# Performance work log

Measured on AMD Instinct MI355X. Metric: run time of the kernel, lower is better.

## Reference

```python
import jax, jax.numpy as jnp
import numpy as np
from jax import lax

B, C, H, W = 2, 3, 512, 512
K = 8                 # kernel_size (= value_patch_size)
G = H // K            # token grid = 64
L = G * G             # 4096 tokens
FD = 128              # feature_dim
PD = C * K * K        # 192 rgb patch dim
MD = PD + FD          # 320 matching token dim
DD = 256              # matching_descriptor_dim
TOPK = 16             # attention_top_k (= reranker_top_k)
RH = 128              # reranker hidden
TEMP = 1.0
NEG = -1e9


def _to_tokens(img):
    # [B,C,H,W] -> [B,L,C*K*K], channel-major patch layout (torch unfold order)
    b = img.shape[0]
    x = img.reshape(b, C, G, K, G, K).transpose(0, 2, 4, 1, 3, 5)
    return x.reshape(b, L, PD)


def _from_tokens(tok):
    # inverse of _to_tokens (non-overlapping fold)
    b = tok.shape[0]
    x = tok.reshape(b, G, G, C, K, K).transpose(0, 3, 1, 4, 2, 5)
    return x.reshape(b, C, H, W)


def setup_inputs() -> dict:
    key = jax.random.key(0)
    ks = jax.random.split(key, 9)
    s = lambda d: 1.0 / np.sqrt(d)
    return {
        "image": jax.random.normal(ks[0], (B, C, H, W), jnp.float32),
        "features": jax.random.normal(ks[1], (B, FD, G, G), jnp.float32),
        "token_mask": jax.random.randint(ks[2], (B, L), 0, 2, jnp.int32),
        "W_desc": jax.random.normal(ks[3], (MD, DD), jnp.float32) * s(MD),
        "Wq_rr": jax.random.normal(ks[4], (MD, RH), jnp.float32) * s(MD),
        "Wk_rr": jax.random.normal(ks[5], (MD, RH), jnp.float32) * s(MD),
        "W1": jax.random.normal(ks[6], (2 * RH + 3, RH), jnp.float32) * s(2 * RH + 3),
        "b1": jnp.zeros((RH,), jnp.float32),
        "W2": jax.random.normal(ks[7], (RH, 1), jnp.float32) * s(RH),
        "b2": jnp.zeros((1,), jnp.float32),
    }


def reference(image, features, token_mask, W_desc, Wq_rr, Wk_rr, W1, b1, W2, b2):
    rgb_tok = _to_tokens(image)                                   # [B,L,192]
    feat_tok = features.reshape(B, FD, L).transpose(0, 2, 1)      # [B,L,128]
    match = jnp.concatenate([rgb_tok, feat_tok], axis=-1)          # [B,L,320]

    # stage-1 matching: descriptor GEMM + scaled dot-product logits
    desc = match @ W_desc                                          # [B,L,256]
    scale = 1.0 / (np.sqrt(DD) * TEMP)
    logits = jnp.einsum("bqd,bkd->bqk", desc, desc) * scale        # [B,L,L]
    key_invalid = token_mask.astype(logits.dtype)                  # 1 = hole
    logits = logits + NEG * key_invalid[:, None, :]

    # top-k candidate selection per query token
    top_logits, top_idx = lax.top_k(logits, TOPK)                  # [B,L,TOPK]

    gather = jax.vmap(lambda m, i: m[i])                            # per-batch gather
    cand = gather(match, top_idx)                                  # [B,L,TOPK,320]

    # relative coordinates on the token grid, normalized
    ys, xs = jnp.meshgrid(jnp.arange(G), jnp.arange(G), indexing="ij")
    pos = jnp.stack([ys.reshape(-1), xs.reshape(-1)], -1).astype(jnp.float32) / G  # [L,2]
    rel = pos[top_idx] - pos[None, :, None, :]                      # [B,L,TOPK,2]

    # reranker MLP over (query, candidate) pairs
    qf = match @ Wq_rr                                              # [B,L,RH]
    kf = cand @ Wk_rr                                               # [B,L,TOPK,RH]
    feats = jnp.concatenate(
        [qf[:, :, None, :] * kf,
         jnp.abs(qf[:, :, None, :] - kf),
         top_logits[..., None],
         rel], axis=-1)                                             # [B,L,TOPK,2RH+3]
    score = (jax.nn.gelu(feats @ W1 + b1, approximate=False) @ W2 + b2)[..., 0]
    refined = top_logits + score                                    # [B,L,TOPK]

    weights = jax.nn.softmax(refined, axis=-1)                      # [B,L,TOPK]

    # gather value patches (value_source='rgb') and blend
    vcand = gather(rgb_tok, top_idx)                                # [B,L,TOPK,192]
    out_tok = jnp.einsum("blk,blkp->blp", weights, vcand)           # [B,L,192]
    out_img = _from_tokens(out_tok)                                 # [B,C,H,W]

    # fusion_mode='replace': replace hole pixels, keep valid pixels
    pix_mask = jnp.repeat(jnp.repeat(token_mask.reshape(B, G, G), K, 1), K, 2)
    pix_mask = pix_mask[:, None, :, :]                              # [B,1,H,W]
    return jnp.where(pix_mask > 0, out_img, image)
```

## Files before the change

kernel.cpp:

```cpp
#include <hip/hip_runtime.h>
#include <hip/hip_bf16.h>
#include <math.h>

#define BB 2
#define CC 3
#define HH 512
#define WW 512
#define GG 64
#define LL 4096
#define FDIM 128
#define PDIM 192
#define MDIM 320
#define DDIM 256
#define TOPK 16
#define RHID 128
#define SCALE (1.0f/16.0f)

#define NQ2 8
#define CHK3 1024
#define KB 2
#define TOKG 16
#define TKT 32
#define NQM 4

__global__ void k_copy_init(const float* __restrict__ img, float* __restrict__ out,
                            int* __restrict__ counts) {
    int i = blockIdx.x * blockDim.x + threadIdx.x;
    if (i < 2 * BB) counts[i] = 0;
    int n4 = BB * CC * HH * WW / 4;
    const float4* s = (const float4*)img;
    float4* d = (float4*)out;
    for (int j = i; j < n4; j += gridDim.x * blockDim.x) d[j] = s[j];
}

__global__ void k_build(const float* __restrict__ img, const float* __restrict__ feat,
                        float* __restrict__ match) {
    int bl = blockIdx.x;
    int b = bl >> 12, l = bl & (LL - 1);
    int gy = l >> 6, gx = l & 63;
    int p = threadIdx.x;
    float v;
    if (p < PDIM) {
        int c = p >> 6, ky = (p >> 3) & 7, kx = p & 7;
        v = img[((b * CC + c) * HH + gy * 8 + ky) * WW + gx * 8 + kx];
    } else {
        v = feat[(b * FDIM + (p - PDIM)) * LL + l];
    }
    match[(size_t)bl * MDIM + p] = v;
}

__global__ void k_compact(const int* __restrict__ mask, int* __restrict__ qlist,
                          int* __restrict__ klist, int* __restrict__ counts) {
    int bl = blockIdx.x * blockDim.x + threadIdx.x;
    if (bl >= BB * LL) return;
    int b = bl >> 12, l = bl & (LL - 1);
    if (mask[bl] > 0) {
        int s = atomicAdd(&counts[b], 1);
        qlist[b * LL + s] = l;
    } else {
        int s = atomicAdd(&counts[BB + b], 1);
        klist[b * LL + s] = l;
    }
}

__global__ __launch_bounds__(256) void k_gemm2(const float* __restrict__ match,
        const float* __restrict__ Wd, const float* __restrict__ Wq,
        const float* __restrict__ Wk,
        float* __restrict__ desc, float* __restrict__ qkf) {
    __shared__ float sm[TOKG * MDIM];
    int base = blockIdx.x * TOKG;
    int t = threadIdx.x;
    for (int i = t; i < TOKG * MDIM; i += 256) sm[i] = match[(size_t)base * MDIM + i];
    __syncthreads();
    const float4* sm4 = (const float4*)sm;
    const float* W1p = (t < 128) ? Wq : Wk;
    int c1 = t & 127;
    float acc0[TOKG], acc1[TOKG];
#pragma unroll
    for (int tt = 0; tt < TOKG; ++tt) { acc0[tt] = 0.f; acc1[tt] = 0.f; }
    for (int m = 0; m < MDIM; m += 4) {
        float w00 = Wd[(m+0)*DDIM + t], w01 = Wd[(m+1)*DDIM + t];
        float w02 = Wd[(m+2)*DDIM + t], w03 = Wd[(m+3)*DDIM + t];
        float w10 = W1p[(m+0)*RHID + c1], w11 = W1p[(m+1)*RHID + c1];
        float w12 = W1p[(m+2)*RHID + c1], w13 = W1p[(m+3)*RHID + c1];
        int mg = m >> 2;
#pragma unroll
        for (int tt = 0; tt < TOKG; ++tt) {
            float4 s = sm4[tt * (MDIM/4) + mg];
            acc0[tt] += s.x*w00 + s.y*w01 + s.z*w02 + s.w*w03;
            acc1[tt] += s.x*w10 + s.y*w11 + s.z*w12 + s.w*w13;
        }
    }
#pragma unroll
    for (int tt = 0; tt < TOKG; ++tt) {
        desc[(size_t)(base+tt)*DDIM + t] = acc0[tt];
        qkf [(size_t)(base+tt)*DDIM + t] = acc1[tt];
    }
}

__global__ __launch_bounds__(256) void k_gatherkT(const float* __restrict__ desc,
        const int* __restrict__ klist, const int* __restrict__ counts,
        float* __restrict__ kdesc_t) {
    int b = blockIdx.y;
    int vcnt = counts[BB + b];
    int kt = blockIdx.x * TKT;
    if (kt >= vcnt) return;
    int nk = min(TKT, vcnt - kt);
    __shared__ float sm[TKT][DDIM + 1];
    int t = threadIdx.x;
    for (int r = (t >> 6); r < nk; r += 4) {
        int src = klist[b * LL + kt + r];
        const float4* s = (const float4*)(desc + ((size_t)b * LL + src) * DDIM);
        float4 v = s[t & 63];
        int d0 = (t & 63) * 4;
        sm[r][d0] = v.x; sm[r][d0+1] = v.y; sm[r][d0+2] = v.z; sm[r][d0+3] = v.w;
    }
    __syncthreads();
    float* outb = kdesc_t + (size_t)b * DDIM * LL;
    int kk = t & 31;
    for (int d = (t >> 5); d < DDIM; d += 8) {
        if (kk < nk) outb[(size_t)d * LL + kt + kk] = sm[kk][d];
    }
}

__global__ __launch_bounds__(256, 4) void k_topk4(const float* __restrict__ desc,
        const float* __restrict__ kdt,
        const int* __restrict__ qlist, const int* __restrict__ klist,
        const int* __restrict__ counts,
        float* __restrict__ tval2, int* __restrict__ tidx2) {
    int b = blockIdx.z;
    int kb = blockIdx.y;
    int cnt  = counts[b];
    int vcnt = counts[BB + b];
    int i0 = blockIdx.x * NQ2;
    if (i0 >= cnt) return;
    int nq = min(NQ2, cnt - i0);
    int t = threadIdx.x;
    int lane = t & 63, w = t >> 6;

    __shared__ float sq[NQ2 * DDIM];
    __shared__ float lc[NQ2][CHK3];

#pragma unroll
    for (int qi = 0; qi < NQ2; ++qi) {
        int qtok = qlist[b * LL + i0 + min(qi, nq - 1)];
        sq[qi * DDIM + t] = desc[((size_t)b * LL + qtok) * DDIM + t];
    }
    __syncthreads();

    int khalf = (vcnt + 1) >> 1;
    int kstart = kb * khalf;
    int kend = min(vcnt, kstart + khalf);

    float tva = -INFINITY, tvb = -INFINITY;
    int   tia = 0x7fffffff, tib = 0x7fffffff;

    const float4* sq4 = (const float4*)sq;
    const float* kbase = kdt + (size_t)b * DDIM * LL;
    const int* klb = klist + b * LL;

    int nch = (kend > kstart) ? (kend - kstart + CHK3 - 1) / CHK3 : 0;
    for (int ch = 0; ch < nch; ++ch) {
        int base = kstart + ch * CHK3;
        int k0 = base + 4 * t;
        int k0c = min(k0, LL - 4);

        float acc[NQ2][4];
#pragma unroll
        for (int qi = 0; qi < NQ2; ++qi)
#pragma unroll
            for (int r = 0; r < 4; ++r) acc[qi][r] = 0.f;

#pragma unroll 2
        for (int db = 0; db < DDIM / 4; ++db) {
            float4 qv[NQ2];
#pragma unroll
            for (int qi = 0; qi < NQ2; ++qi) qv[qi] = sq4[qi * (DDIM/4) + db];
#pragma unroll
            for (int dd = 0; dd < 4; ++dd) {
                float4 kx = *(const float4*)(kbase + (size_t)(db * 4 + dd) * LL + k0c);
#pragma unroll
                for (int qi = 0; qi < NQ2; ++qi) {
                    float sv = (dd == 0) ? qv[qi].x : (dd == 1) ? qv[qi].y
                             : (dd == 2) ? qv[qi].z : qv[qi].w;
                    acc[qi][0] += sv * kx.x;
                    acc[qi][1] += sv * kx.y;
                    acc[qi][2] += sv * kx.z;
                    acc[qi][3] += sv * kx.w;
                }
            }
        }
        __syncthreads();
#pragma unroll
        for (int qi = 0; qi < NQ2; ++qi) {
            float4 o;
            o.x = (k0 + 0 < kend) ? acc[qi][0] * SCALE : -INFINITY;
            o.y = (k0 + 1 < kend) ? acc[qi][1] * SCALE : -INFINITY;
            o.z = (k0 + 2 < kend) ? acc[qi][2] * SCALE : -INFINITY;
            o.w = (k0 + 3 < kend) ? acc[qi][3] * SCALE : -INFINITY;
            *(float4*)&lc[qi][4 * t] = o;
        }
        __syncthreads();

        auto select_q = [&](float& tv, int& ti, int qi) {
            for (int j = 0; j < CHK3 / 64; ++j) {
                int p = j * 64 + lane;
                int gk = base + p;
                float v = lc[qi][p];
                int kidx = (gk < kend) ? klb[gk] : 0x7fffffff;
                float thrv = __shfl(tv, 15);
                int   thri = __shfl(ti, 15);
                bool pass = (v > thrv) || (v == thrv && kidx < thri);
                unsigned long long mball = __ballot(pass);
                while (mball) {
                    int src = __ffsll(mball) - 1;
                    float vv = __shfl(v, src);
                    int   ii = __shfl(kidx, src);
                    bool beat = (vv > tv) || (vv == tv && ii < ti);
                    float pv = __shfl_up(tv, 1);
                    int   pi = __shfl_up(ti, 1);
                    bool beatp = (lane > 0) && ((vv > pv) || (vv == pv && ii < pi));
                    if (lane < 16 && beat) { tv = beatp ? pv : vv; ti = beatp ? pi : ii; }
                    mball &= mball - 1;
                    if (mball) {
                        float t15 = __shfl(tv, 15);
                        int   i15 = __shfl(ti, 15);
                        bool still = (v > t15) || (v == t15 && kidx < i15);
                        mball &= __ballot(still);
                    }
                }
            }
        };
        select_q(tva, tia, 2 * w + 0);
        select_q(tvb, tib, 2 * w + 1);
    }

#pragma unroll
    for (int qq = 0; qq < 2; ++qq) {
        int qi = w * 2 + qq;
        float tv = qq ? tvb : tva;
        int   ti = qq ? tib : tia;
        if (qi < nq && lane < 16) {
            size_t o = (((size_t)b * LL + i0 + qi) * KB + kb) * TOPK + lane;
            tval2[o] = tv;
            tidx2[o] = ti;
        }
    }
}

__device__ __forceinline__ float gelu_f(float x) {
    return 0.5f * x * (1.0f + erff(x * 0.70710678118654752f));
}

__global__ __launch_bounds__(256, 4) void k_mlp2(const float* __restrict__ match,
        const float* __restrict__ qkf,
        const float* __restrict__ tval2, const int* __restrict__ tidx2,
        const int* __restrict__ qlist, const int* __restrict__ counts,
        const float* __restrict__ W1, const float* __restrict__ b1,
        const float* __restrict__ W2, const float* __restrict__ b2,
        float* __restrict__ out) {
    int b = blockIdx.y;
    int cnt = counts[b];
    int i0 = blockIdx.x * NQM;
    if (i0 >= cnt) return;
    int t = threadIdx.x;
    int ql = t >> 6;
    int lane = t & 63;
    int rt = lane >> 4;
    int ht = lane & 15;
    int h0 = ht * 8;
    int k0 = rt * 4;

    __shared__ float mv[NQM][32];
    __shared__ int   mi[NQM][32];
    __shared__ float tl[NQM][16];
    __shared__ int   tix[NQM][16];
    __shared__ float rr0[NQM][16], rr1[NQM][16];
    __shared__ int   qtok[NQM];
    __shared__ float qf[NQM][128];
    __shared__ float kf[64][132];
    __shared__ float wgt[NQM][16];

    if (t < NQM) qtok[t] = qlist[b * LL + min(i0 + t, cnt - 1)];
    if (t < NQM * 32) {
        int q = t >> 5, u = t & 31;
        size_t o = (((size_t)b * LL + min(i0 + q, cnt - 1)) * KB + (u >> 4)) * TOPK + (u & 15);
        mv[q][u] = tval2[o];
        mi[q][u] = tidx2[o];
    }
    __syncthreads();
    if (t < NQM * 32) {
        int q = t >> 5, u = t & 31;
        float v = mv[q][u]; int ii = mi[q][u];
        int rank = 0;
#pragma unroll 1
        for (int x = 0; x < 32; ++x) {
            float vx = mv[q][x]; int ix = mi[q][x];
            rank += ((vx > v) || (vx == v && (ix < ii || (ix == ii && x < u)))) ? 1 : 0;
        }
        if (rank < TOPK) {
            int kidx = (ii < 0 || ii >= LL) ? 0 : ii;
            tl[q][rank] = v;
            tix[q][rank] = kidx;
            int qt = qtok[q];
            rr0[q][rank] = (float)((kidx >> 6) - (qt >> 6)) * (1.0f / GG);
            rr1[q][rank] = (float)((kidx & 63) - (qt & 63)) * (1.0f / GG);
        }
    }
    __syncthreads();
    for (int idx = t; idx < NQM * 128; idx += 256) {
        int q = idx >> 7, d = idx & 127;
        qf[q][d] = qkf[((size_t)b * LL + qtok[q]) * DDIM + d];
    }
    for (int idx = t; idx < 64 * 128; idx += 256) {
        int row = idx >> 7, d = idx & 127;
        kf[row][d] = qkf[((size_t)b * LL + tix[row >> 4][row & 15]) * DDIM + 128 + d];
    }
    __syncthreads();

    float acc[4][8];
#pragma unroll
    for (int i = 0; i < 4; ++i)
#pragma unroll
        for (int h = 0; h < 8; ++h) acc[i][h] = 0.f;

    const float4* W14 = (const float4*)W1;
    const float* qfr = qf[ql];
    const float* kfr0 = &kf[ql * 16 + k0][0];
    for (int j = 0; j < 128; ++j) {
        float qv = qfr[j];
        int ca = (j * RHID + h0) >> 2;
        int cb = ((RHID + j) * RHID + h0) >> 2;
        float4 wa0 = W14[ca], wa1 = W14[ca + 1];
        float4 wb0 = W14[cb], wb1 = W14[cb + 1];
#pragma unroll
        for (int i = 0; i < 4; ++i) {
            float kv = kfr0[i * 132 + j];
            float pa = qv * kv;
            float pb = fabsf(qv - kv);
            acc[i][0] += pa * wa0.x + pb * wb0.x;
            acc[i][1] += pa * wa0.y + pb * wb0.y;
            acc[i][2] += pa * wa0.z + pb * wb0.z;
            acc[i][3] += pa * wa0.w + pb * wb0.w;
            acc[i][4] += pa * wa1.x + pb * wb1.x;
            acc[i][5] += pa * wa1.y + pb * wb1.y;
            acc[i][6] += pa * wa1.z + pb * wb1.z;
            acc[i][7] += pa * wa1.w + pb * wb1.w;
        }
    }

    int cl = (256 * RHID + h0) >> 2;
    int cr0 = (257 * RHID + h0) >> 2;
    int cr1 = (258 * RHID + h0) >> 2;
    float4 wl0 = W14[cl], wl1 = W14[cl + 1];
    float4 wra = W14[cr0], wrb = W14[cr0 + 1];
    float4 wsa = W14[cr1], wsb = W14[cr1 + 1];
    float4 bb0 = ((const float4*)b1)[h0 >> 2], bb1v = ((const float4*)b1)[(h0 >> 2) + 1];
    float4 w20 = ((const float4*)W2)[h0 >> 2], w21 = ((const float4*)W2)[(h0 >> 2) + 1];
    float b2v = b2[0];

    float scv0, scv1, scv2, scv3;
    {
#pragma unroll
        for (int i = 0; i < 4; ++i) {
            int k = k0 + i;
            float tlv = tl[ql][k], r0v = rr0[ql][k], r1v = rr1[ql][k];
            float s = 0.f;
            s += gelu_f(acc[i][0] + tlv*wl0.x + r0v*wra.x + r1v*wsa.x + bb0.x) * w20.x;
            s += gelu_f(acc[i][1] + tlv*wl0.y + r0v*wra.y + r1v*wsa.y + bb0.y) * w20.y;
            s += gelu_f(acc[i][2] + tlv*wl0.z + r0v*wra.z + r1v*wsa.z + bb0.z) * w20.z;
            s += gelu_f(acc[i][3] + tlv*wl0.w + r0v*wra.w + r1v*wsa.w + bb0.w) * w20.w;
            s += gelu_f(acc[i][4] + tlv*wl1.x + r0v*wrb.x + r1v*wsb.x + bb1v.x) * w21.x;
            s += gelu_f(acc[i][5] + tlv*wl1.y + r0v*wrb.y + r1v*wsb.y + bb1v.y) * w21.y;
            s += gelu_f(acc[i][6] + tlv*wl1.z + r0v*wrb.z + r1v*wsb.z + bb1v.z) * w21.z;
            s += gelu_f(acc[i][7] + tlv*wl1.w + r0v*wrb.w + r1v*wsb.w + bb1v.w) * w21.w;
            s += __shfl_xor(s, 1); s += __shfl_xor(s, 2);
            s += __shfl_xor(s, 4); s += __shfl_xor(s, 8);
            if (i == 0) scv0 = s; else if (i == 1) scv1 = s;
            else if (i == 2) scv2 = s; else scv3 = s;
        }
    }
    if (ht == 0) {
        wgt[ql][k0 + 0] = scv0;
        wgt[ql][k0 + 1] = scv1;
        wgt[ql][k0 + 2] = scv2;
        wgt[ql][k0 + 3] = scv3;
    }
    __syncthreads();
    if (lane < 16) {
        float refined = tl[ql][lane] + wgt[ql][lane] + b2v;
        float m = refined;
        for (int off = 8; off > 0; off >>= 1) m = fmaxf(m, __shfl_xor(m, off, 16));
        float e = expf(refined - m);
        float s = e;
        for (int off = 8; off > 0; off >>= 1) s += __shfl_xor(s, off, 16);
        wgt[ql][lane] = e / s;
    }
    __syncthreads();
    int gyq = qtok[ql] >> 6, gxq = qtok[ql] & 63;
    for (int p = lane; p < PDIM; p += 64) {
        float o = 0.f;
#pragma unroll
        for (int k = 0; k < TOPK; ++k)
            o += wgt[ql][k] * match[((size_t)b * LL + tix[ql][k]) * MDIM + p];
        int c = p >> 6, ky = (p >> 3) & 7, kx = p & 7;
        out[((b * CC + c) * HH + gyq * 8 + ky) * WW + gxq * 8 + kx] = o;
    }
}

extern "C" void kernel_launch(void* const* d_in, const int* in_sizes, int n_in,
                              void* d_out, int out_size, void* d_ws, size_t ws_size,
                              hipStream_t stream) {
    const float* image    = (const float*)d_in[0];
    const float* features = (const float*)d_in[1];
    const int*   tmask    = (const int*)d_in[2];
    const float* W_desc   = (const float*)d_in[3];
    const float* Wq       = (const float*)d_in[4];
    const float* Wk       = (const float*)d_in[5];
    const float* W1       = (const float*)d_in[6];
    const float* b1       = (const float*)d_in[7];
    const float* W2       = (const float*)d_in[8];
    const float* b2       = (const float*)d_in[9];
    float* out = (float*)d_out;

    float* ws    = (float*)d_ws;
    float* match = ws;
    float* desc  = match + (size_t)BB * LL * MDIM;
    float* qkf   = desc  + (size_t)BB * LL * DDIM;
    float* kdt   = qkf   + (size_t)BB * LL * DDIM;
    float* tval2 = kdt   + (size_t)BB * DDIM * LL;
    int*   tidx2 = (int*)(tval2 + (size_t)BB * LL * KB * TOPK);
    int*   qlist = tidx2 + (size_t)BB * LL * KB * TOPK;
    int*   klist = qlist + BB * LL;
    int*   counts = klist + BB * LL;

    k_copy_init<<<1024, 256, 0, stream>>>(image, out, counts);
    k_build<<<BB * LL, MDIM, 0, stream>>>(image, features, match);
    k_compact<<<(BB * LL + 255) / 256, 256, 0, stream>>>(tmask, qlist, klist, counts);
    k_gemm2<<<BB * LL / TOKG, 256, 0, stream>>>(match, W_desc, Wq, Wk, desc, qkf);
    k_gatherkT<<<dim3(LL / TKT, BB), 256, 0, stream>>>(desc, klist, counts, kdt);
    k_topk4<<<dim3(LL / NQ2, KB, BB), 256, 0, stream>>>(desc, kdt, qlist, klist,
                                                        counts, tval2, tidx2);
    k_mlp2<<<dim3(LL / NQM, BB), 256, 0, stream>>>(match, qkf, tval2, tidx2, qlist,
                                                   counts, W1, b1, W2, b2, out);
}
```

Measured before the change: 412.7 us.

## Select top-k per wavefront from registers, merge eight partial lists in MLP

Drops the shared-memory logit staging and its two block barriers in the top-k kernel. Each wavefront now keeps a running top-16 for all eight queries straight from its accumulator registers, and the unscaled scores are scaled once at write-out. The output becomes eight partial lists per query (two key halves times four wavefronts) instead of two. The MLP kernel then merges 128 candidates per query with an O(n²) rank count, which adds merge work and more register state per thread.

```diff
diff --git a/kernel.cpp b/kernel.cpp
--- a/kernel.cpp
+++ b/kernel.cpp
@@ -19,6 +19,7 @@
 #define NQ2 8
 #define CHK3 1024
 #define KB 2
+#define NL 8
 #define TOKG 16
 #define TKT 32
 #define NQM 4
@@ -123,11 +124,11 @@
     }
 }
 
-__global__ __launch_bounds__(256, 4) void k_topk4(const float* __restrict__ desc,
+__global__ __launch_bounds__(256, 4) void k_topk8(const float* __restrict__ desc,
         const float* __restrict__ kdt,
         const int* __restrict__ qlist, const int* __restrict__ klist,
         const int* __restrict__ counts,
-        float* __restrict__ tval2, int* __restrict__ tidx2) {
+        float* __restrict__ tval3, int* __restrict__ tidx3) {
     int b = blockIdx.z;
     int kb = blockIdx.y;
     int cnt  = counts[b];
@@ -139,7 +140,6 @@
     int lane = t & 63, w = t >> 6;
 
     __shared__ float sq[NQ2 * DDIM];
-    __shared__ float lc[NQ2][CHK3];
 
 #pragma unroll
     for (int qi = 0; qi < NQ2; ++qi) {
@@ -152,8 +152,9 @@
     int kstart = kb * khalf;
     int kend = min(vcnt, kstart + khalf);
 
-    float tva = -INFINITY, tvb = -INFINITY;
-    int   tia = 0x7fffffff, tib = 0x7fffffff;
+    float tvv[NQ2]; int tii[NQ2];
+#pragma unroll
+    for (int q = 0; q < NQ2; ++q) { tvv[q] = -INFINITY; tii[q] = 0x7fffffff; }
 
     const float4* sq4 = (const float4*)sq;
     const float* kbase = kdt + (size_t)b * DDIM * LL;
@@ -190,27 +191,20 @@
                 }
             }
         }
-        __syncthreads();
-#pragma unroll
-        for (int qi = 0; qi < NQ2; ++qi) {
-            float4 o;
-            o.x = (k0 + 0 < kend) ? acc[qi][0] * SCALE : -INFINITY;
-            o.y = (k0 + 1 < kend) ? acc[qi][1] * SCALE : -INFINITY;
-            o.z = (k0 + 2 < kend) ? acc[qi][2] * SCALE : -INFINITY;
-            o.w = (k0 + 3 < kend) ? acc[qi][3] * SCALE : -INFINITY;
-            *(float4*)&lc[qi][4 * t] = o;
-        }
-        __syncthreads();
-
-        auto select_q = [&](float& tv, int& ti, int qi) {
-            for (int j = 0; j < CHK3 / 64; ++j) {
-                int p = j * 64 + lane;
-                int gk = base + p;
-                float v = lc[qi][p];
-                int kidx = (gk < kend) ? klb[gk] : 0x7fffffff;
-                float thrv = __shfl(tv, 15);
-                int   thri = __shfl(ti, 15);
-                bool pass = (v > thrv) || (v == thrv && kidx < thri);
+
+        int4 kid4 = *(const int4*)(klb + k0c);
+#pragma unroll
+        for (int q = 0; q < NQ2; ++q) {
+            float tv = tvv[q]; int ti = tii[q];
+            float thrv = __shfl(tv, 15);
+            int   thri = __shfl(ti, 15);
+#pragma unroll
+            for (int r = 0; r < 4; ++r) {
+                float v = acc[q][r];
+                int kidx = (r == 0) ? kid4.x : (r == 1) ? kid4.y
+                         : (r == 2) ? kid4.z : kid4.w;
+                bool valid = (k0 + r < kend);
+                bool pass = valid && ((v > thrv) || (v == thrv && kidx < thri));
                 unsigned long long mball = __ballot(pass);
                 while (mball) {
                     int src = __ffsll(mball) - 1;
@@ -222,28 +216,27 @@
                     bool beatp = (lane > 0) && ((vv > pv) || (vv == pv && ii < pi));
                     if (lane < 16 && beat) { tv = beatp ? pv : vv; ti = beatp ? pi : ii; }
                     mball &= mball - 1;
+                    thrv = __shfl(tv, 15);
+                    thri = __shfl(ti, 15);
                     if (mball) {
-                        float t15 = __shfl(tv, 15);
-                        int   i15 = __shfl(ti, 15);
-                        bool still = (v > t15) || (v == t15 && kidx < i15);
+                        bool still = valid && ((v > thrv) || (v == thrv && kidx < thri));
                         mball &= __ballot(still);
                     }
                 }
             }
-        };
-        select_q(tva, tia, 2 * w + 0);
-        select_q(tvb, tib, 2 * w + 1);
-    }
-
-#pragma unroll
-    for (int qq = 0; qq < 2; ++qq) {
-        int qi = w * 2 + qq;
-        float tv = qq ? tvb : tva;
-        int   ti = qq ? tib : tia;
-        if (qi < nq && lane < 16) {
-            size_t o = (((size_t)b * LL + i0 + qi) * KB + kb) * TOPK + lane;
-            tval2[o] = tv;
-            tidx2[o] = ti;
+            tvv[q] = tv; tii[q] = ti;
+        }
+    }
+
+    if (lane < 16) {
+        int li = kb * 4 + w;
+#pragma unroll
+        for (int q = 0; q < NQ2; ++q) {
+            if (q < nq) {
+                size_t o = (((size_t)b * LL + i0 + q) * NL + li) * TOPK + lane;
+                tval3[o] = tvv[q] * SCALE;
+                tidx3[o] = tii[q];
+            }
         }
     }
 }
@@ -254,7 +247,7 @@
 
 __global__ __launch_bounds__(256, 4) void k_mlp2(const float* __restrict__ match,
         const float* __restrict__ qkf,
-        const float* __restrict__ tval2, const int* __restrict__ tidx2,
+        const float* __restrict__ tval3, const int* __restrict__ tidx3,
         const int* __restrict__ qlist, const int* __restrict__ counts,
         const float* __restrict__ W1, const float* __restrict__ b1,
         const float* __restrict__ W2, const float* __restrict__ b2,
@@ -271,8 +264,8 @@
     int h0 = ht * 8;
     int k0 = rt * 4;
 
-    __shared__ float mv[NQM][32];
-    __shared__ int   mi[NQM][32];
+    __shared__ float mv[NQM][NL * TOPK];
+    __shared__ int   mi[NQM][NL * TOPK];
     __shared__ float tl[NQM][16];
     __shared__ int   tix[NQM][16];
     __shared__ float rr0[NQM][16], rr1[NQM][16];
@@ -282,19 +275,19 @@
     __shared__ float wgt[NQM][16];
 
     if (t < NQM) qtok[t] = qlist[b * LL + min(i0 + t, cnt - 1)];
-    if (t < NQM * 32) {
-        int q = t >> 5, u = t & 31;
-        size_t o = (((size_t)b * LL + min(i0 + q, cnt - 1)) * KB + (u >> 4)) * TOPK + (u & 15);
-        mv[q][u] = tval2[o];
-        mi[q][u] = tidx2[o];
-    }
-    __syncthreads();
-    if (t < NQM * 32) {
-        int q = t >> 5, u = t & 31;
+    for (int e = t; e < NQM * NL * TOPK; e += 256) {
+        int q = e >> 7, u = e & 127;
+        size_t o = (((size_t)b * LL + min(i0 + q, cnt - 1)) * NL + (u >> 4)) * TOPK + (u & 15);
+        mv[q][u] = tval3[o];
+        mi[q][u] = tidx3[o];
+    }
+    __syncthreads();
+    for (int e = t; e < NQM * NL * TOPK; e += 256) {
+        int q = e >> 7, u = e & 127;
         float v = mv[q][u]; int ii = mi[q][u];
         int rank = 0;
 #pragma unroll 1
-        for (int x = 0; x < 32; ++x) {
+        for (int x = 0; x < NL * TOPK; ++x) {
             float vx = mv[q][x]; int ix = mi[q][x];
             rank += ((vx > v) || (vx == v && (ix < ii || (ix == ii && x < u)))) ? 1 : 0;
         }
@@ -428,9 +421,9 @@
     float* desc  = match + (size_t)BB * LL * MDIM;
     float* qkf   = desc  + (size_t)BB * LL * DDIM;
     float* kdt   = qkf   + (size_t)BB * LL * DDIM;
-    float* tval2 = kdt   + (size_t)BB * DDIM * LL;
-    int*   tidx2 = (int*)(tval2 + (size_t)BB * LL * KB * TOPK);
-    int*   qlist = tidx2 + (size_t)BB * LL * KB * TOPK;
+    float* tval3 = kdt   + (size_t)BB * DDIM * LL;
+    int*   tidx3 = (int*)(tval3 + (size_t)BB * LL * NL * TOPK);
+    int*   qlist = tidx3 + (size_t)BB * LL * NL * TOPK;
     int*   klist = qlist + BB * LL;
     int*   counts = klist + BB * LL;
 
@@ -439,8 +432,8 @@
     k_compact<<<(BB * LL + 255) / 256, 256, 0, stream>>>(tmask, qlist, klist, counts);
     k_gemm2<<<BB * LL / TOKG, 256, 0, stream>>>(match, W_desc, Wq, Wk, desc, qkf);
     k_gatherkT<<<dim3(LL / TKT, BB), 256, 0, stream>>>(desc, klist, counts, kdt);
-    k_topk4<<<dim3(LL / NQ2, KB, BB), 256, 0, stream>>>(desc, kdt, qlist, klist,
-                                                        counts, tval2, tidx2);
-    k_mlp2<<<dim3(LL / NQM, BB), 256, 0, stream>>>(match, qkf, tval2, tidx2, qlist,
+    k_topk8<<<dim3(LL / NQ2, KB, BB), 256, 0, stream>>>(desc, kdt, qlist, klist,
+                                                        counts, tval3, tidx3);
+    k_mlp2<<<dim3(LL / NQM, BB), 256, 0, stream>>>(match, qkf, tval3, tidx3, qlist,
                                                    counts, W1, b1, W2, b2, out);
 }
```

Measured after the change: 548.7 us. 1.33x slower.
